# Kernel tuning notes

Hardware: AMD Instinct MI355X
Metric: run time of the kernel (lower is better)

## Reference

```python
import jax, jax.numpy as jnp
import numpy as np

B, S, D = 4, 2048, 1024
D_K, D_V = 1024, 1024


def setup_inputs() -> dict:
    key = jax.random.key(0)
    ks = jax.random.split(key, 9)
    s = 1.0 / np.sqrt(D)
    return {
        "q_in": jax.random.normal(ks[0], (B, S, D), jnp.float32),
        "k_in": jax.random.normal(ks[1], (B, S, D), jnp.float32),
        "v_in": jax.random.normal(ks[2], (B, S, D), jnp.float32),
        "Wq": jax.random.normal(ks[3], (D, D_K), jnp.float32) * s,
        "bq": jnp.zeros((D_K,), jnp.float32),
        "Wk": jax.random.normal(ks[4], (D, D_K), jnp.float32) * s,
        "bk": jnp.zeros((D_K,), jnp.float32),
        "Wv": jax.random.normal(ks[5], (D, D_V), jnp.float32) * s,
        "bv": jnp.zeros((D_V,), jnp.float32),
    }


def reference(q_in, k_in, v_in, Wq, bq, Wk, bk, Wv, bv):
    q = jnp.einsum("bsd,dk->bsk", q_in, Wq) + bq  # [B,S,d_k]
    k = jnp.einsum("bsd,dk->bsk", k_in, Wk) + bk  # [B,S,d_k]
    v = jnp.einsum("bsd,dv->bsv", v_in, Wv) + bv  # [B,S,d_v]
    scores = jnp.einsum("bqk,bsk->bqs", q, k) / jnp.sqrt(jnp.float32(D_K))
    attn = jax.nn.softmax(scores, axis=-1)  # [B,S,S]
    return jnp.einsum("bqs,bsv->bqv", attn, v)
```

## Files before the change

### kernel.cpp

```cpp
#include <hip/hip_runtime.h>
#include <stdint.h>

#define B_  4
#define S_  2048
#define D_  1024
#define DK_ 1024
#define DV_ 1024

typedef __attribute__((ext_vector_type(8)))  short short8;
typedef __attribute__((ext_vector_type(16))) float floatx16;

#define ASYNC16(gsrc, ldst)                                                        \
  __builtin_amdgcn_global_load_lds(                                                \
      (const __attribute__((address_space(1))) unsigned int*)(gsrc),               \
      (__attribute__((address_space(3))) unsigned int*)(ldst), 16, 0, 0)

#define WAITVM(N) asm volatile("s_waitcnt vmcnt(" #N ")" ::: "memory")

__device__ __forceinline__ unsigned short f2bf(float f) {
  union { float f; uint32_t u; } v; v.f = f;
  uint32_t r = v.u + 0x7fffu + ((v.u >> 16) & 1u);
  return (unsigned short)(r >> 16);
}

__global__ __launch_bounds__(256)
void prep(const float* __restrict__ q, const float* __restrict__ k, const float* __restrict__ v,
          const float* __restrict__ W0, const float* __restrict__ W1, const float* __restrict__ W2,
          unsigned short* __restrict__ qkv, unsigned short* __restrict__ WT) {
  const int bid = blockIdx.x, tid = threadIdx.x;
  if (bid < 12288) {
    const int t  = bid >> 12;
    const int cb = bid & 4095;
    const float* in = (t == 0) ? q : (t == 1) ? k : v;
    unsigned short* o = qkv + (long)t * ((long)B_ * S_ * D_);
    const int i0 = cb * 512 + tid;
    float4 v0 = ((const float4*)in)[i0];
    float4 v1 = ((const float4*)in)[i0 + 256];
    ushort4 u0, u1;
    u0.x = f2bf(v0.x); u0.y = f2bf(v0.y); u0.z = f2bf(v0.z); u0.w = f2bf(v0.w);
    u1.x = f2bf(v1.x); u1.y = f2bf(v1.y); u1.z = f2bf(v1.z); u1.w = f2bf(v1.w);
    ((ushort4*)o)[i0] = u0;
    ((ushort4*)o)[i0 + 256] = u1;
  } else {
    const int b2 = bid - 12288;
    const int w  = b2 >> 10;
    const int tl = b2 & 1023;
    const float* in = (w == 0) ? W0 : (w == 1) ? W1 : W2;
    unsigned short* o = WT + (long)w * D_ * DK_;
    __shared__ float tile[32][33];
    const int bx = (tl & 31) * 32, by = (tl >> 5) * 32;
    const int tx = tid & 31, ty = tid >> 5;
    for (int r = ty; r < 32; r += 8)
      tile[r][tx] = in[(long)(by + r) * DK_ + bx + tx];
    __syncthreads();
    for (int r = ty; r < 32; r += 8)
      o[(long)(bx + r) * D_ + by + tx] = f2bf(tile[tx][r]);
  }
}

__device__ __forceinline__ void storeC(float* p, float v)          { *p = v; }
__device__ __forceinline__ void storeC(unsigned short* p, float v) { *p = f2bf(v); }

template <typename OutT, int NOUT, int MODE, int KSPL>
__global__ __launch_bounds__(512, 2)
void gemm_bt256(const unsigned short* __restrict__ A0, const unsigned short* __restrict__ A1,
                const unsigned short* __restrict__ A2, const unsigned short* __restrict__ Bm,
                OutT* __restrict__ C0, OutT* __restrict__ C1, OutT* __restrict__ C2,
                const float* __restrict__ b0, const float* __restrict__ b1,
                const float* __restrict__ b2, float* __restrict__ rowsum,
                int N, int K, int lda, int ldb, long sA, long sB, long sC, float scale) {
  __shared__ __align__(16) unsigned short As[2][256 * 64];
  __shared__ __align__(16) unsigned short Bs[2][256 * 64];
  __shared__ float invs[256];
  const int tid  = threadIdx.x;
  const int lane = tid & 63, wave = tid >> 6;
  const int wm = (wave >> 2) * 128;
  const int wn = (wave & 3) * 64;
  const int lm = lane & 31;
  const int hi = lane >> 5;

  const int gx = gridDim.x, gy = gridDim.y;
  const int T  = gx * gy * (int)gridDim.z;
  const int l  = blockIdx.x + gx * (blockIdx.y + gy * blockIdx.z);
  const int l2 = (l & 7) * (T >> 3) + (l >> 3);
  const int bxi = l2 % gx;
  const int byi = (l2 / gx) % gy;
  const int bzi = l2 / (gx * gy);

  const int  kh = (KSPL > 1) ? (bzi & (KSPL - 1)) : 0;
  const long zb = (KSPL > 1) ? (bzi >> 1) : bzi;
  const int m0  = byi * 256;
  const int n0g = bxi * 256;

  const unsigned short* A = A0;
  OutT* C = C0;
  const float* bias = b0;
  int n0 = n0g, sel = 0;
  if (NOUT == 3) {
    sel = n0g >> 10;
    n0 = n0g & 1023;
    if (sel == 1)      { A = A1; C = C1; bias = b1; }
    else if (sel == 2) { A = A2; C = C2; bias = b2; }
  }
  A += zb * sA + (long)kh * K;
  const unsigned short* Bp = Bm + zb * sB + (long)kh * K;
  C += zb * sC;

  const int srow  = lane >> 3;
  const int sslot = ((lane & 7) ^ srow) * 8;
  const unsigned short* gA = A  + (long)(m0  + 32 * wave + srow) * lda + sslot;
  const unsigned short* gB = Bp + (long)(n0g + 32 * wave + srow) * ldb + sslot;
  const int lb = wave * 2048;

  floatx16 acc[4][2] = {};
  const int swz = lm & 7;

  const int nt = K >> 6;

#pragma unroll
  for (int a = 0; a < 4; a++) ASYNC16(gA + (long)(8 * a) * lda, &As[0][lb + a * 512]);
#pragma unroll
  for (int a = 0; a < 4; a++) ASYNC16(gB + (long)(8 * a) * ldb, &Bs[0][lb + a * 512]);
  gA += 64; gB += 64;
  WAITVM(0);
  __builtin_amdgcn_s_barrier();

  for (int t = 0; t < nt; t++) {
    const int p = t & 1;
    const bool pre = (t + 1 < nt);
#pragma unroll
    for (int q = 0; q < 4; q++) {
      const int i0 = (q >> 1) * 2;
      const int s0 = (q & 1) * 2;
      short8 af[2][2], bf[2][2];
#pragma unroll
      for (int i = 0; i < 2; i++)
#pragma unroll
        for (int s = 0; s < 2; s++)
          af[i][s] = *(const short8*)
            &As[p][(wm + (i0 + i) * 32 + lm) * 64 + ((((s0 + s) * 2 + hi) ^ swz) * 8)];
#pragma unroll
      for (int j = 0; j < 2; j++)
#pragma unroll
        for (int s = 0; s < 2; s++)
          bf[j][s] = *(const short8*)
            &Bs[p][(wn + j * 32 + lm) * 64 + ((((s0 + s) * 2 + hi) ^ swz) * 8)];
      if (q == 0 && pre) {
#pragma unroll
        for (int a = 0; a < 4; a++) ASYNC16(gA + (long)(8 * a) * lda, &As[p ^ 1][lb + a * 512]);
      }
      if (q == 1 && pre) {
#pragma unroll
        for (int a = 0; a < 4; a++) ASYNC16(gB + (long)(8 * a) * ldb, &Bs[p ^ 1][lb + a * 512]);
        gA += 64; gB += 64;
      }
      __builtin_amdgcn_s_barrier();
      asm volatile("s_waitcnt lgkmcnt(0)" ::: "memory");
      __builtin_amdgcn_s_setprio(1);
#pragma unroll
      for (int s = 0; s < 2; s++)
#pragma unroll
        for (int i = 0; i < 2; i++)
#pragma unroll
          for (int j = 0; j < 2; j++)
            acc[i0 + i][j] =
                __builtin_amdgcn_mfma_f32_32x32x16_bf16(af[i][s], bf[j][s], acc[i0 + i][j], 0, 0, 0);
      __builtin_amdgcn_s_setprio(0);
      if (q == 3) WAITVM(0);
      __builtin_amdgcn_s_barrier();
    }
  }

  if (MODE == 2 || MODE == 3) {
    __syncthreads();
    if (tid < 256) invs[tid] = 1.0f / rowsum[zb * S_ + m0 + tid];
    __syncthreads();
  }

  if (NOUT == 3 && sel == 2) {
    unsigned short* Vt = (unsigned short*)C;
    const int b = m0 >> 11;
    const int sbase = (m0 & 2047);
#pragma unroll
    for (int i = 0; i < 4; i++) {
      const int srowb = sbase + wm + i * 32 + (hi << 2);
#pragma unroll
      for (int j = 0; j < 2; j++) {
        const int col = n0 + wn + j * 32 + lm;
        const float bv = bias[col];
        unsigned short* vp = Vt + ((long)b * DV_ + col) * S_ + srowb;
#pragma unroll
        for (int g = 0; g < 4; g++) {
          ushort4 u;
          u.x = f2bf(acc[i][j][4 * g + 0] + bv);
          u.y = f2bf(acc[i][j][4 * g + 1] + bv);
          u.z = f2bf(acc[i][j][4 * g + 2] + bv);
          u.w = f2bf(acc[i][j][4 * g + 3] + bv);
          *(ushort4*)(vp + 8 * g) = u;
        }
      }
    }
  } else if (MODE == 1) {
#pragma unroll
    for (int i = 0; i < 4; i++) {
#pragma unroll
      for (int r = 0; r < 16; r++) {
        const int row = m0 + wm + i * 32 + (r & 3) + ((r >> 2) << 3) + (hi << 2);
        float sum2 = 0.f;
#pragma unroll
        for (int j = 0; j < 2; j++) {
          const int col = n0 + wn + j * 32 + lm;
          float e = __expf(acc[i][j][r] * scale);
          storeC(C + (long)row * N + col, e);
          sum2 += e;
        }
#pragma unroll
        for (int msk = 1; msk < 32; msk <<= 1) sum2 += __shfl_xor(sum2, msk, 64);
        if ((lane & 31) == 0) atomicAdd(&rowsum[zb * S_ + row], sum2);
      }
    }
  } else {
#pragma unroll
    for (int i = 0; i < 4; i++) {
#pragma unroll
      for (int j = 0; j < 2; j++) {
        const int col = n0 + wn + j * 32 + lm;
        const float bv = bias ? bias[col] : 0.f;
#pragma unroll
        for (int r = 0; r < 16; r++) {
          const int rl = wm + i * 32 + (r & 3) + ((r >> 2) << 3) + (hi << 2);
          float val = acc[i][j][r] * scale + bv;
          if (MODE == 3) {
            atomicAdd((float*)(C + (long)(m0 + rl) * N + col), val * invs[rl]);
          } else {
            if (MODE == 2) val *= invs[rl];
            storeC(C + (long)(m0 + rl) * N + col, val);
          }
        }
      }
    }
  }
}

extern "C" void kernel_launch(void* const* d_in, const int* in_sizes, int n_in,
                              void* d_out, int out_size, void* d_ws, size_t ws_size,
                              hipStream_t stream) {
  const float* q_in = (const float*)d_in[0];
  const float* k_in = (const float*)d_in[1];
  const float* v_in = (const float*)d_in[2];
  const float* Wq   = (const float*)d_in[3];
  const float* bq   = (const float*)d_in[4];
  const float* Wk   = (const float*)d_in[5];
  const float* bk   = (const float*)d_in[6];
  const float* Wv   = (const float*)d_in[7];
  const float* bv   = (const float*)d_in[8];
  float* out = (float*)d_out;

  char* ws = (char*)d_ws;
  const long nX = (long)B_ * S_ * D_;
  const long nW = (long)D_ * DK_;
  unsigned short* qb  = (unsigned short*)(ws);
  unsigned short* kb  = qb + nX;
  unsigned short* vb  = kb + nX;
  unsigned short* WqT = vb + nX;
  unsigned short* Qb  = WqT + 3 * nW;
  unsigned short* Kb  = Qb + nX;
  unsigned short* Vt  = Kb + nX;
  float*          rowsum = (float*)(Vt + nX);
  unsigned short* U   = (unsigned short*)ws;

  dim3 blk(256), blk5(512);

  hipMemsetAsync(rowsum, 0, (size_t)B_ * S_ * sizeof(float), stream);
  hipMemsetAsync(out, 0, (size_t)B_ * S_ * DV_ * sizeof(float), stream);

  {
    dim3 g(12288 + 3072);
    prep<<<g, blk, 0, stream>>>(q_in, k_in, v_in, Wq, Wk, Wv, qb, WqT);
  }
  {
    dim3 g(3 * DK_ / 256, (B_ * S_) / 256, 1);
    gemm_bt256<unsigned short, 3, 0, 1><<<g, blk5, 0, stream>>>(
        qb, kb, vb, WqT, Qb, Kb, Vt, bq, bk, bv, nullptr,
        DK_, D_, D_, D_, 0, 0, 0, 1.f);
  }
  {
    dim3 g(S_ / 256, S_ / 256, B_);
    gemm_bt256<unsigned short, 1, 1, 1><<<g, blk5, 0, stream>>>(
        Qb, nullptr, nullptr, Kb, U, nullptr, nullptr, nullptr, nullptr, nullptr, rowsum,
        S_, DK_, DK_, DK_, (long)S_ * DK_, (long)S_ * DK_, (long)S_ * S_, 0.03125f);
  }
  {
    dim3 g(DV_ / 256, S_ / 256, B_ * 2);
    gemm_bt256<float, 1, 3, 2><<<g, blk5, 0, stream>>>(
        U, nullptr, nullptr, Vt, out, nullptr, nullptr, nullptr, nullptr, nullptr, rowsum,
        DV_, S_ / 2, S_, S_, (long)S_ * S_, (long)DV_ * S_, (long)S_ * DV_, 1.f);
  }
}
```

Before: 377.2 us.

## Switch GEMM mainloop to triple-buffered 32-wide K tiles with two-stage prefetch

```diff
diff --git a/kernel.cpp b/kernel.cpp
--- a/kernel.cpp
+++ b/kernel.cpp
@@ -69,8 +69,8 @@
                 const float* __restrict__ b0, const float* __restrict__ b1,
                 const float* __restrict__ b2, float* __restrict__ rowsum,
                 int N, int K, int lda, int ldb, long sA, long sB, long sC, float scale) {
-  __shared__ __align__(16) unsigned short As[2][256 * 64];
-  __shared__ __align__(16) unsigned short Bs[2][256 * 64];
+  __shared__ __align__(16) unsigned short As[3][256 * 32];
+  __shared__ __align__(16) unsigned short Bs[3][256 * 32];
   __shared__ float invs[256];
   const int tid  = threadIdx.x;
   const int lane = tid & 63, wave = tid >> 6;
@@ -106,69 +106,85 @@
   const unsigned short* Bp = Bm + zb * sB + (long)kh * K;
   C += zb * sC;
 
-  const int srow  = lane >> 3;
-  const int sslot = ((lane & 7) ^ srow) * 8;
-  const unsigned short* gA = A  + (long)(m0  + 32 * wave + srow) * lda + sslot;
-  const unsigned short* gB = Bp + (long)(n0g + 32 * wave + srow) * ldb + sslot;
-  const int lb = wave * 2048;
+  const int rr = lane >> 2;
+  const int cc = (((lane & 3) ^ ((lane >> 3) & 3)) * 8);
+  const unsigned short* gA0 = A  + (long)(m0  + 32 * wave + rr) * lda + cc;
+  const unsigned short* gA1 = gA0 + 16 * (long)lda;
+  const unsigned short* gB0 = Bp + (long)(n0g + 32 * wave + rr) * ldb + cc;
+  const unsigned short* gB1 = gB0 + 16 * (long)ldb;
+  const int la0 = wave * 1024, la1 = wave * 1024 + 512;
 
   floatx16 acc[4][2] = {};
-  const int swz = lm & 7;
-
-  const int nt = K >> 6;
-
-#pragma unroll
-  for (int a = 0; a < 4; a++) ASYNC16(gA + (long)(8 * a) * lda, &As[0][lb + a * 512]);
-#pragma unroll
-  for (int a = 0; a < 4; a++) ASYNC16(gB + (long)(8 * a) * ldb, &Bs[0][lb + a * 512]);
-  gA += 64; gB += 64;
-  WAITVM(0);
+  const int sw = (lm >> 1) & 3;
+
+  const int nt = K >> 5;
+
+  ASYNC16(gA0, &As[0][la0]); ASYNC16(gA1, &As[0][la1]);
+  ASYNC16(gB0, &Bs[0][la0]); ASYNC16(gB1, &Bs[0][la1]);
+  gA0 += 32; gA1 += 32; gB0 += 32; gB1 += 32;
+  ASYNC16(gA0, &As[1][la0]); ASYNC16(gA1, &As[1][la1]);
+  ASYNC16(gB0, &Bs[1][la0]); ASYNC16(gB1, &Bs[1][la1]);
+  gA0 += 32; gA1 += 32; gB0 += 32; gB1 += 32;
+  WAITVM(4);
   __builtin_amdgcn_s_barrier();
 
+  int bc = 0;
   for (int t = 0; t < nt; t++) {
-    const int p = t & 1;
-    const bool pre = (t + 1 < nt);
-#pragma unroll
-    for (int q = 0; q < 4; q++) {
-      const int i0 = (q >> 1) * 2;
-      const int s0 = (q & 1) * 2;
-      short8 af[2][2], bf[2][2];
+    const int bs = (bc + 2 >= 3) ? bc - 1 : bc + 2;
+    const bool pre = (t + 2 < nt);
+
+    short8 af[2][2], bf[2][2];
+#pragma unroll
+    for (int i = 0; i < 2; i++)
+#pragma unroll
+      for (int s = 0; s < 2; s++)
+        af[i][s] = *(const short8*)&As[bc][(wm + i * 32 + lm) * 32 + (((s * 2 + hi) ^ sw) * 8)];
+#pragma unroll
+    for (int j = 0; j < 2; j++)
+#pragma unroll
+      for (int s = 0; s < 2; s++)
+        bf[j][s] = *(const short8*)&Bs[bc][(wn + j * 32 + lm) * 32 + (((s * 2 + hi) ^ sw) * 8)];
+    if (pre) {
+      ASYNC16(gA0, &As[bs][la0]); ASYNC16(gA1, &As[bs][la1]);
+      gA0 += 32; gA1 += 32;
+    }
+    __builtin_amdgcn_s_barrier();
+    asm volatile("s_waitcnt lgkmcnt(0)" ::: "memory");
+    __builtin_amdgcn_s_setprio(1);
+#pragma unroll
+    for (int s = 0; s < 2; s++)
 #pragma unroll
       for (int i = 0; i < 2; i++)
 #pragma unroll
-        for (int s = 0; s < 2; s++)
-          af[i][s] = *(const short8*)
-            &As[p][(wm + (i0 + i) * 32 + lm) * 64 + ((((s0 + s) * 2 + hi) ^ swz) * 8)];
-#pragma unroll
-      for (int j = 0; j < 2; j++)
-#pragma unroll
-        for (int s = 0; s < 2; s++)
-          bf[j][s] = *(const short8*)
-            &Bs[p][(wn + j * 32 + lm) * 64 + ((((s0 + s) * 2 + hi) ^ swz) * 8)];
-      if (q == 0 && pre) {
-#pragma unroll
-        for (int a = 0; a < 4; a++) ASYNC16(gA + (long)(8 * a) * lda, &As[p ^ 1][lb + a * 512]);
-      }
-      if (q == 1 && pre) {
-#pragma unroll
-        for (int a = 0; a < 4; a++) ASYNC16(gB + (long)(8 * a) * ldb, &Bs[p ^ 1][lb + a * 512]);
-        gA += 64; gB += 64;
-      }
-      __builtin_amdgcn_s_barrier();
-      asm volatile("s_waitcnt lgkmcnt(0)" ::: "memory");
-      __builtin_amdgcn_s_setprio(1);
+        for (int j = 0; j < 2; j++)
+          acc[i][j] = __builtin_amdgcn_mfma_f32_32x32x16_bf16(af[i][s], bf[j][s], acc[i][j], 0, 0, 0);
+    __builtin_amdgcn_s_setprio(0);
+    __builtin_amdgcn_s_barrier();
+
+    short8 af2[2][2];
+#pragma unroll
+    for (int i = 0; i < 2; i++)
 #pragma unroll
       for (int s = 0; s < 2; s++)
-#pragma unroll
-        for (int i = 0; i < 2; i++)
-#pragma unroll
-          for (int j = 0; j < 2; j++)
-            acc[i0 + i][j] =
-                __builtin_amdgcn_mfma_f32_32x32x16_bf16(af[i][s], bf[j][s], acc[i0 + i][j], 0, 0, 0);
-      __builtin_amdgcn_s_setprio(0);
-      if (q == 3) WAITVM(0);
-      __builtin_amdgcn_s_barrier();
-    }
+        af2[i][s] = *(const short8*)&As[bc][(wm + (2 + i) * 32 + lm) * 32 + (((s * 2 + hi) ^ sw) * 8)];
+    if (pre) {
+      ASYNC16(gB0, &Bs[bs][la0]); ASYNC16(gB1, &Bs[bs][la1]);
+      gB0 += 32; gB1 += 32;
+    }
+    __builtin_amdgcn_s_barrier();
+    asm volatile("s_waitcnt lgkmcnt(0)" ::: "memory");
+    __builtin_amdgcn_s_setprio(1);
+#pragma unroll
+    for (int s = 0; s < 2; s++)
+#pragma unroll
+      for (int i = 0; i < 2; i++)
+#pragma unroll
+        for (int j = 0; j < 2; j++)
+          acc[2 + i][j] = __builtin_amdgcn_mfma_f32_32x32x16_bf16(af2[i][s], bf[j][s], acc[2 + i][j], 0, 0, 0);
+    __builtin_amdgcn_s_setprio(0);
+    if (pre) { WAITVM(4); } else { WAITVM(0); }
+    __builtin_amdgcn_s_barrier();
+    bc = (bc == 2) ? 0 : bc + 1;
   }
 
   if (MODE == 2 || MODE == 3) {
```

New measurement: 374.0 us. About the same (-0.8%).
